# Performance work log

Measured on AMD Instinct MI355X. Metric: run time of the kernel, lower is better.

The kernel has to match this reference:

```python
import jax, jax.numpy as jnp
import numpy as np

N = 100000      # nodes
E = 1600000     # edges
IN_DIM = 500
HID = 64
OUT = 40
BN_EPS = 1e-5


def setup_inputs() -> dict:
    key = jax.random.key(0)
    ks = jax.random.split(key, 20)
    x = jax.random.normal(ks[0], (N, IN_DIM), dtype=jnp.float32)
    edge_index = jax.random.randint(ks[1], (2, E), 0, N, dtype=jnp.int64)

    def lin(k, fin, fout):
        return jax.random.normal(k, (fin, fout), dtype=jnp.float32) / np.sqrt(fin).astype(np.float32)

    inp = {
        "x": x,
        "edge_index": edge_index,
        "W1": lin(ks[2], IN_DIM, HID),
        "b1": jnp.zeros((HID,), jnp.float32),
        "g1": jnp.ones((HID,), jnp.float32),
        "be1": jnp.zeros((HID,), jnp.float32),
        "m1": 0.1 * jax.random.normal(ks[3], (HID,), jnp.float32),
        "v1": jax.random.uniform(ks[4], (HID,), jnp.float32, 0.5, 1.5),
        "W2": lin(ks[5], HID, HID),
        "b2": jnp.zeros((HID,), jnp.float32),
        "g2": jnp.ones((HID,), jnp.float32),
        "be2": jnp.zeros((HID,), jnp.float32),
        "m2": 0.1 * jax.random.normal(ks[6], (HID,), jnp.float32),
        "v2": jax.random.uniform(ks[7], (HID,), jnp.float32, 0.5, 1.5),
        "W3": lin(ks[8], HID, OUT),
        "b3": jnp.zeros((OUT,), jnp.float32),
    }
    return inp


def _gcn_conv(h, src, dst, deg_inv_sqrt, W, b):
    # PyG GCNConv (add_self_loops=True, normalize=True, eval math):
    # out = D^-1/2 (A + I) D^-1/2 (h @ W) + b
    h = h @ W                                    # [N, F]
    norm = deg_inv_sqrt[src] * deg_inv_sqrt[dst]  # [E]
    msg = h[src] * norm[:, None]                  # [E, F] gather
    agg = jax.ops.segment_sum(msg, dst, num_segments=N)  # scatter-add
    agg = agg + h * (deg_inv_sqrt * deg_inv_sqrt)[:, None]  # self-loop term
    return agg + b


def reference(x, edge_index, W1, b1, g1, be1, m1, v1,
              W2, b2, g2, be2, m2, v2, W3, b3):
    src, dst = edge_index[0], edge_index[1]
    # degree including self-loop
    deg = jax.ops.segment_sum(jnp.ones((E,), x.dtype), dst, num_segments=N) + 1.0
    deg_inv_sqrt = jax.lax.rsqrt(deg)

    def bn(h, g, be, m, v):
        return (h - m) * jax.lax.rsqrt(v + BN_EPS) * g + be

    h = _gcn_conv(x, src, dst, deg_inv_sqrt, W1, b1)
    h = jax.nn.relu(bn(h, g1, be1, m1, v1))
    # dropout: identity in eval mode
    h = _gcn_conv(h, src, dst, deg_inv_sqrt, W2, b2)
    h = jax.nn.relu(bn(h, g2, be2, m2, v2))
    out = _gcn_conv(h, src, dst, deg_inv_sqrt, W3, b3)
    return jax.nn.log_softmax(out, axis=1)
```

## Files before the change

kernel.cpp:

```cpp
#include <hip/hip_runtime.h>
#include <math.h>

#define N_NODES 100000
#define N_EDGES 1600000
#define IN_DIM  500
#define HID     64
#define OUT_DIM 40
#define BN_EPS  1e-5f
#define SCAN_NB 98
#define NTILE   6250

typedef __attribute__((ext_vector_type(8))) short bf16x8;
typedef __attribute__((ext_vector_type(4))) float f32x4;

static inline int cdiv(long a, int b) { return (int)((a + b - 1) / b); }

__device__ inline unsigned short f2bf_rne(float f) {
    unsigned int u = __float_as_uint(f);
    unsigned int r = (u + 0x7FFFu + ((u >> 16) & 1u)) >> 16;
    return (unsigned short)r;
}

__global__ void k_zero2(int* a, int* b) {
    int i = blockIdx.x * 256 + threadIdx.x;
    if (i < N_NODES) { a[i] = 0; b[i] = 0; }
}

__global__ void k_count_deg(const int* __restrict__ ei, int* degi) {
    int e = blockIdx.x * 256 + threadIdx.x;
    if (e < N_EDGES) atomicAdd(&degi[ei[N_EDGES + e]], 1);
}

__global__ void k_dis(const int* __restrict__ degi, float* dis) {
    int i = blockIdx.x * 256 + threadIdx.x;
    if (i < N_NODES) dis[i] = rsqrtf((float)degi[i] + 1.0f);
}

__global__ void k_scan1(const int* __restrict__ degi, int* __restrict__ rowptr,
                        int* __restrict__ blocksum) {
    __shared__ int sd[256];
    int tid = threadIdx.x;
    int base = blockIdx.x * 1024 + tid * 4;
    int v0 = (base + 0 < N_NODES) ? degi[base + 0] : 0;
    int v1 = (base + 1 < N_NODES) ? degi[base + 1] : 0;
    int v2 = (base + 2 < N_NODES) ? degi[base + 2] : 0;
    int v3 = (base + 3 < N_NODES) ? degi[base + 3] : 0;
    int s = v0 + v1 + v2 + v3;
    sd[tid] = s;
    __syncthreads();
    for (int off = 1; off < 256; off <<= 1) {
        int t = (tid >= off) ? sd[tid - off] : 0;
        __syncthreads();
        sd[tid] += t;
        __syncthreads();
    }
    int excl = sd[tid] - s;
    if (base + 0 < N_NODES) rowptr[base + 0] = excl;
    if (base + 1 < N_NODES) rowptr[base + 1] = excl + v0;
    if (base + 2 < N_NODES) rowptr[base + 2] = excl + v0 + v1;
    if (base + 3 < N_NODES) rowptr[base + 3] = excl + v0 + v1 + v2;
    if (tid == 255) blocksum[blockIdx.x] = sd[255];
}

__global__ void k_scan2(int* __restrict__ blocksum, int* __restrict__ blockbase) {
    __shared__ int sd[128];
    int tid = threadIdx.x;
    int v = (tid < SCAN_NB) ? blocksum[tid] : 0;
    sd[tid] = v;
    __syncthreads();
    for (int off = 1; off < 128; off <<= 1) {
        int t = (tid >= off) ? sd[tid - off] : 0;
        __syncthreads();
        sd[tid] += t;
        __syncthreads();
    }
    if (tid < SCAN_NB) blockbase[tid] = sd[tid] - v;
}

__global__ void k_scan3(int* __restrict__ rowptr, const int* __restrict__ blockbase) {
    int add = blockbase[blockIdx.x];
    int base = blockIdx.x * 1024 + threadIdx.x * 4;
#pragma unroll
    for (int i = 0; i < 4; ++i)
        if (base + i < N_NODES) rowptr[base + i] += add;
}

__global__ void k_permute(const int* __restrict__ ei, const int* __restrict__ rowptr,
                          int* __restrict__ cursor, const float* __restrict__ dis,
                          uint2* __restrict__ epack) {
    int e = blockIdx.x * 256 + threadIdx.x;
    if (e >= N_EDGES) return;
    int s = ei[e];
    int d = ei[N_EDGES + e];
    int pos = rowptr[d] + atomicAdd(&cursor[d], 1);
    epack[pos] = make_uint2((unsigned int)(s * 128),
                            __float_as_uint(dis[s] * dis[d]));
}

template <int K, int F, int T>
__global__ void k_convWp(const float* __restrict__ W, unsigned short* __restrict__ wb) {
    int idx = blockIdx.x * 256 + threadIdx.x;
    if (idx >= T * 2048) return;
    int j    = idx & 7;
    int lane = (idx >> 3) & 63;
    int q    = idx >> 9;
    int t    = q >> 2, nt = q & 3;
    int n = nt * 16 + (lane & 15);
    int k = t * 32 + ((lane >> 4) << 3) + j;
    float v = (k < K && n < F) ? W[(long)k * F + n] : 0.f;
    wb[idx] = f2bf_rne(v);
}

__global__ __launch_bounds__(256) void k_l1fused(
        const float* __restrict__ x,
        const unsigned short* __restrict__ wb,
        unsigned short* __restrict__ h) {
    __shared__ unsigned short l[16 * 520];
    const int rt = blockIdx.x;
    const int tid = threadIdx.x;

#pragma unroll
    for (int it = 0; it < 8; ++it) {
        int slot = it * 256 + tid;
        int row = slot >> 7, kq = slot & 127;
        float4 v = make_float4(0.f, 0.f, 0.f, 0.f);
        if (kq < 125)
            v = *reinterpret_cast<const float4*>(x + ((long)rt * 16 + row) * IN_DIM + kq * 4);
        unsigned int u0 = (unsigned int)f2bf_rne(v.x) | ((unsigned int)f2bf_rne(v.y) << 16);
        unsigned int u1 = (unsigned int)f2bf_rne(v.z) | ((unsigned int)f2bf_rne(v.w) << 16);
        *reinterpret_cast<uint2*>(&l[row * 520 + kq * 4]) = make_uint2(u0, u1);
    }
    __syncthreads();

    const int wid  = tid >> 6;
    const int lane = tid & 63;
    const int l15  = lane & 15;
    const int lhi  = lane >> 4;

    const bf16x8* bp = reinterpret_cast<const bf16x8*>(wb) + wid * 64 + lane;
    const unsigned short* arow = &l[l15 * 520 + lhi * 8];

    f32x4 acc = (f32x4){0.f, 0.f, 0.f, 0.f};
    bf16x8 ca = *reinterpret_cast<const bf16x8*>(arow);
    bf16x8 cb = bp[0];

#pragma unroll
    for (int t = 0; t < 16; ++t) {
        bf16x8 na, nb;
        if (t < 15) {
            na = *reinterpret_cast<const bf16x8*>(arow + (t + 1) * 32);
            nb = bp[(t + 1) * 256];
        }
        acc = __builtin_amdgcn_mfma_f32_16x16x32_bf16(ca, cb, acc, 0, 0, 0);
        if (t < 15) { ca = na; cb = nb; }
    }

#pragma unroll
    for (int rr = 0; rr < 4; ++rr) {
        long grow = (long)rt * 16 + lhi * 4 + rr;
        h[grow * 64 + wid * 16 + l15] = f2bf_rne(acc[rr]);
    }
}

template <int T>
__global__ __launch_bounds__(256) void k_gemm_packed(
        const unsigned short* __restrict__ xp,
        const unsigned short* __restrict__ wb,
        unsigned short* __restrict__ h) {
    const int tid  = threadIdx.x;
    const int wid  = tid >> 6;
    const int lane = tid & 63;
    const int rt   = blockIdx.x * 4 + wid;
    if (rt >= NTILE) return;

    const bf16x8* ap = reinterpret_cast<const bf16x8*>(xp) + (long)rt * T * 64 + lane;
    const bf16x8* bp = reinterpret_cast<const bf16x8*>(wb) + lane;

    f32x4 acc[4];
#pragma unroll
    for (int nt = 0; nt < 4; ++nt) acc[nt] = (f32x4){0.f, 0.f, 0.f, 0.f};

    bf16x8 ca = ap[0];
    bf16x8 cb0 = bp[0], cb1 = bp[64], cb2 = bp[128], cb3 = bp[192];

    for (int t = 0; t < T; ++t) {
        bf16x8 na, nb0, nb1, nb2, nb3;
        if (t + 1 < T) {
            na  = ap[(t + 1) * 64];
            nb0 = bp[((t + 1) * 4 + 0) * 64];
            nb1 = bp[((t + 1) * 4 + 1) * 64];
            nb2 = bp[((t + 1) * 4 + 2) * 64];
            nb3 = bp[((t + 1) * 4 + 3) * 64];
        }
        acc[0] = __builtin_amdgcn_mfma_f32_16x16x32_bf16(ca, cb0, acc[0], 0, 0, 0);
        acc[1] = __builtin_amdgcn_mfma_f32_16x16x32_bf16(ca, cb1, acc[1], 0, 0, 0);
        acc[2] = __builtin_amdgcn_mfma_f32_16x16x32_bf16(ca, cb2, acc[2], 0, 0, 0);
        acc[3] = __builtin_amdgcn_mfma_f32_16x16x32_bf16(ca, cb3, acc[3], 0, 0, 0);
        if (t + 1 < T) { ca = na; cb0 = nb0; cb1 = nb1; cb2 = nb2; cb3 = nb3; }
    }

    const int l15 = lane & 15, lhi = lane >> 4;
#pragma unroll
    for (int nt = 0; nt < 4; ++nt) {
        int coln = nt * 16 + l15;
#pragma unroll
        for (int rr = 0; rr < 4; ++rr) {
            long grow = (long)rt * 16 + lhi * 4 + rr;
            h[grow * 64 + coln] = f2bf_rne(acc[nt][rr]);
        }
    }
}

__global__ __launch_bounds__(256) void k_agg_bn_relu(
        const unsigned short* __restrict__ h, const int* __restrict__ rowptr,
        const int* __restrict__ degi, const uint2* __restrict__ epack,
        const float* __restrict__ dis,
        const float* __restrict__ bias, const float* __restrict__ g,
        const float* __restrict__ be, const float* __restrict__ m,
        const float* __restrict__ v, unsigned short* __restrict__ xp_out) {
    int node = blockIdx.x * 4 + (threadIdx.x >> 6);
    if (node >= N_NODES) return;
    const int lane = threadIdx.x & 63;
    const int e8 = lane >> 3, c8 = lane & 7;

    const int start = rowptr[node];
    const int cnt   = degi[node];
    const uint2* ep = epack + start;
    const char*  hb = (const char*)h + c8 * 16;

    float a[8] = {0.f, 0.f, 0.f, 0.f, 0.f, 0.f, 0.f, 0.f};

    auto batch = [&](int j) {
        int jj = j + e8;
        bool valid = jj < cnt;
        uint2 mv = ep[valid ? jj : 0];
        float w = valid ? __uint_as_float(mv.y) : 0.0f;
        uint4 hv = *(const uint4*)(hb + mv.x);
        a[0] += __uint_as_float(hv.x << 16) * w;
        a[1] += __uint_as_float(hv.x & 0xffff0000u) * w;
        a[2] += __uint_as_float(hv.y << 16) * w;
        a[3] += __uint_as_float(hv.y & 0xffff0000u) * w;
        a[4] += __uint_as_float(hv.z << 16) * w;
        a[5] += __uint_as_float(hv.z & 0xffff0000u) * w;
        a[6] += __uint_as_float(hv.w << 16) * w;
        a[7] += __uint_as_float(hv.w & 0xffff0000u) * w;
    };

    int j = 0;
    for (; j + 8 < cnt; j += 16) { batch(j); batch(j + 8); }
    if (j < cnt) batch(j);

#pragma unroll
    for (int i = 0; i < 8; ++i) {
        a[i] += __shfl_xor(a[i], 8);
        a[i] += __shfl_xor(a[i], 16);
        a[i] += __shfl_xor(a[i], 32);
    }

    if (e8 == 0) {
        float d = dis[node], d2 = d * d;
        uint4 sv = *(const uint4*)((const char*)h + (long)node * 128 + c8 * 16);
        float sf[8] = {
            __uint_as_float(sv.x << 16), __uint_as_float(sv.x & 0xffff0000u),
            __uint_as_float(sv.y << 16), __uint_as_float(sv.y & 0xffff0000u),
            __uint_as_float(sv.z << 16), __uint_as_float(sv.z & 0xffff0000u),
            __uint_as_float(sv.w << 16), __uint_as_float(sv.w & 0xffff0000u)};
        float4 bb0 = *(const float4*)(bias + c8 * 8), bb1 = *(const float4*)(bias + c8 * 8 + 4);
        float4 mm0 = *(const float4*)(m + c8 * 8),    mm1 = *(const float4*)(m + c8 * 8 + 4);
        float4 vv0 = *(const float4*)(v + c8 * 8),    vv1 = *(const float4*)(v + c8 * 8 + 4);
        float4 gg0 = *(const float4*)(g + c8 * 8),    gg1 = *(const float4*)(g + c8 * 8 + 4);
        float4 ee0 = *(const float4*)(be + c8 * 8),   ee1 = *(const float4*)(be + c8 * 8 + 4);
        float bbv[8] = {bb0.x, bb0.y, bb0.z, bb0.w, bb1.x, bb1.y, bb1.z, bb1.w};
        float mmv[8] = {mm0.x, mm0.y, mm0.z, mm0.w, mm1.x, mm1.y, mm1.z, mm1.w};
        float vvv[8] = {vv0.x, vv0.y, vv0.z, vv0.w, vv1.x, vv1.y, vv1.z, vv1.w};
        float ggv[8] = {gg0.x, gg0.y, gg0.z, gg0.w, gg1.x, gg1.y, gg1.z, gg1.w};
        float eev[8] = {ee0.x, ee0.y, ee0.z, ee0.w, ee1.x, ee1.y, ee1.z, ee1.w};

        unsigned int u[4];
#pragma unroll
        for (int p = 0; p < 4; ++p) {
            float r0 = a[2 * p]     + sf[2 * p]     * d2 + bbv[2 * p];
            float r1 = a[2 * p + 1] + sf[2 * p + 1] * d2 + bbv[2 * p + 1];
            r0 = fmaxf((r0 - mmv[2 * p])     * rsqrtf(vvv[2 * p]     + BN_EPS) * ggv[2 * p]     + eev[2 * p],     0.f);
            r1 = fmaxf((r1 - mmv[2 * p + 1]) * rsqrtf(vvv[2 * p + 1] + BN_EPS) * ggv[2 * p + 1] + eev[2 * p + 1], 0.f);
            u[p] = (unsigned int)f2bf_rne(r0) | ((unsigned int)f2bf_rne(r1) << 16);
        }

        int n16 = node & 15, rt2 = node >> 4;
        long base = (((long)rt2 * 2 + (c8 >> 2)) * 64 + (c8 & 3) * 16 + n16) * 8;
        *reinterpret_cast<uint4*>(xp_out + base) = make_uint4(u[0], u[1], u[2], u[3]);
    }
}

__global__ __launch_bounds__(256) void k_agg_lsm(
        const unsigned short* __restrict__ h, const int* __restrict__ rowptr,
        const int* __restrict__ degi, const uint2* __restrict__ epack,
        const float* __restrict__ dis,
        const float* __restrict__ bias, float* __restrict__ out) {
    int node = blockIdx.x * 4 + (threadIdx.x >> 6);
    if (node >= N_NODES) return;
    const int lane = threadIdx.x & 63;
    const int e8 = lane >> 3, c8 = lane & 7;

    const int start = rowptr[node];
    const int cnt   = degi[node];
    const uint2* ep = epack + start;
    const char*  hb = (const char*)h + c8 * 16;

    float a[8] = {0.f, 0.f, 0.f, 0.f, 0.f, 0.f, 0.f, 0.f};

    auto batch = [&](int j) {
        int jj = j + e8;
        bool valid = jj < cnt;
        uint2 mv = ep[valid ? jj : 0];
        float w = valid ? __uint_as_float(mv.y) : 0.0f;
        uint4 hv = *(const uint4*)(hb + mv.x);
        a[0] += __uint_as_float(hv.x << 16) * w;
        a[1] += __uint_as_float(hv.x & 0xffff0000u) * w;
        a[2] += __uint_as_float(hv.y << 16) * w;
        a[3] += __uint_as_float(hv.y & 0xffff0000u) * w;
        a[4] += __uint_as_float(hv.z << 16) * w;
        a[5] += __uint_as_float(hv.z & 0xffff0000u) * w;
        a[6] += __uint_as_float(hv.w << 16) * w;
        a[7] += __uint_as_float(hv.w & 0xffff0000u) * w;
    };

    int j = 0;
    for (; j + 8 < cnt; j += 16) { batch(j); batch(j + 8); }
    if (j < cnt) batch(j);

#pragma unroll
    for (int i = 0; i < 8; ++i) {
        a[i] += __shfl_xor(a[i], 8);
        a[i] += __shfl_xor(a[i], 16);
        a[i] += __shfl_xor(a[i], 32);
    }

    const bool ok = c8 < 5;
    float d = dis[node], d2 = d * d;
    uint4 sv = *(const uint4*)((const char*)h + (long)node * 128 + c8 * 16);
    float sf[8] = {
        __uint_as_float(sv.x << 16), __uint_as_float(sv.x & 0xffff0000u),
        __uint_as_float(sv.y << 16), __uint_as_float(sv.y & 0xffff0000u),
        __uint_as_float(sv.z << 16), __uint_as_float(sv.z & 0xffff0000u),
        __uint_as_float(sv.w << 16), __uint_as_float(sv.w & 0xffff0000u)};
    float vals[8];
    float mx = -INFINITY;
    if (ok) {
        float4 bb0 = *(const float4*)(bias + c8 * 8), bb1 = *(const float4*)(bias + c8 * 8 + 4);
        float bbv[8] = {bb0.x, bb0.y, bb0.z, bb0.w, bb1.x, bb1.y, bb1.z, bb1.w};
#pragma unroll
        for (int i = 0; i < 8; ++i) {
            vals[i] = a[i] + sf[i] * d2 + bbv[i];
            mx = fmaxf(mx, vals[i]);
        }
    }
#pragma unroll
    for (int o = 1; o < 8; o <<= 1) mx = fmaxf(mx, __shfl_xor(mx, o));
    float es = 0.f;
    if (ok) {
#pragma unroll
        for (int i = 0; i < 8; ++i) es += expf(vals[i] - mx);
    }
#pragma unroll
    for (int o = 1; o < 8; o <<= 1) es += __shfl_xor(es, o);
    float ls = logf(es);

    if (e8 == 0 && ok) {
        float* op = out + (long)node * 40 + c8 * 8;
        *(float4*)op = make_float4(vals[0] - mx - ls, vals[1] - mx - ls,
                                   vals[2] - mx - ls, vals[3] - mx - ls);
        *(float4*)(op + 4) = make_float4(vals[4] - mx - ls, vals[5] - mx - ls,
                                         vals[6] - mx - ls, vals[7] - mx - ls);
    }
}

extern "C" void kernel_launch(void* const* d_in, const int* in_sizes, int n_in,
                              void* d_out, int out_size, void* d_ws, size_t ws_size,
                              hipStream_t stream) {
    const float* x   = (const float*)d_in[0];
    const int*   ei  = (const int*)d_in[1];
    const float* W1  = (const float*)d_in[2];
    const float* b1  = (const float*)d_in[3];
    const float* g1  = (const float*)d_in[4];
    const float* be1 = (const float*)d_in[5];
    const float* m1  = (const float*)d_in[6];
    const float* v1  = (const float*)d_in[7];
    const float* W2  = (const float*)d_in[8];
    const float* b2  = (const float*)d_in[9];
    const float* g2  = (const float*)d_in[10];
    const float* be2 = (const float*)d_in[11];
    const float* m2  = (const float*)d_in[12];
    const float* v2  = (const float*)d_in[13];
    const float* W3  = (const float*)d_in[14];
    const float* b3  = (const float*)d_in[15];
    float* out = (float*)d_out;

    float* ws        = (float*)d_ws;
    float* dis       = ws;
    int*   degi      = (int*)(ws + 100096);
    int*   cursor    = (int*)(ws + 200192);
    int*   rowptr    = (int*)(ws + 300288);
    int*   blocksum  = (int*)(ws + 400384);
    int*   blockbase = (int*)(ws + 400512);
    uint2* epack     = (uint2*)(ws + 400640);
    unsigned short* bufH = (unsigned short*)(ws + 3600640);
    unsigned short* xp2  = (unsigned short*)(ws + 32400640);
    unsigned short* xp3  = (unsigned short*)(ws + 35600640);
    unsigned short* wb1  = (unsigned short*)(ws + 38800640);
    unsigned short* wb2  = (unsigned short*)(ws + 38817024);
    unsigned short* wb3  = (unsigned short*)(ws + 38819072);

    k_zero2<<<cdiv(N_NODES, 256), 256, 0, stream>>>(degi, cursor);
    k_count_deg<<<cdiv(N_EDGES, 256), 256, 0, stream>>>(ei, degi);
    k_dis<<<cdiv(N_NODES, 256), 256, 0, stream>>>(degi, dis);
    k_scan1<<<SCAN_NB, 256, 0, stream>>>(degi, rowptr, blocksum);
    k_scan2<<<1, 128, 0, stream>>>(blocksum, blockbase);
    k_scan3<<<SCAN_NB, 256, 0, stream>>>(rowptr, blockbase);
    k_permute<<<cdiv(N_EDGES, 256), 256, 0, stream>>>(ei, rowptr, cursor, dis, epack);

    k_convWp<IN_DIM, HID, 16><<<128, 256, 0, stream>>>(W1, wb1);
    k_convWp<HID, HID, 2><<<16, 256, 0, stream>>>(W2, wb2);
    k_convWp<HID, OUT_DIM, 2><<<16, 256, 0, stream>>>(W3, wb3);

    const int gemm_grid = cdiv(NTILE, 4);
    const int agg_grid  = cdiv(N_NODES, 4);

    k_l1fused<<<NTILE, 256, 0, stream>>>(x, wb1, bufH);
    k_agg_bn_relu<<<agg_grid, 256, 0, stream>>>(bufH, rowptr, degi, epack,
                                                dis, b1, g1, be1, m1, v1, xp2);

    k_gemm_packed<2><<<gemm_grid, 256, 0, stream>>>(xp2, wb2, bufH);
    k_agg_bn_relu<<<agg_grid, 256, 0, stream>>>(bufH, rowptr, degi, epack,
                                                dis, b2, g2, be2, m2, v2, xp3);

    k_gemm_packed<2><<<gemm_grid, 256, 0, stream>>>(xp3, wb3, bufH);
    k_agg_lsm<<<agg_grid, 256, 0, stream>>>(bufH, rowptr, degi, epack,
                                            dis, b3, out);
}
```

Before: 400.8 us.

## Switch bf16 to fp16 with packed half2 aggregation and fuse small setup kernels

Replaces the bf16 storage and MFMA with fp16 throughout. The edge aggregation now accumulates in packed half2 FMA instead of unpacking to fp32, and edge weights are stored as duplicated halves. Separately, the degree-inverse-sqrt computation is folded into the scan, the zeroing kernel becomes a memset, and the three weight-conversion launches are merged into one. This cuts ALU work in the gather loop and launch count, but fp16 accumulation over neighbours and the fp16 range limit on raw inputs add precision and overflow risk.

```diff
diff --git a/kernel.cpp b/kernel.cpp
--- a/kernel.cpp
+++ b/kernel.cpp
@@ -10,20 +10,19 @@
 #define SCAN_NB 98
 #define NTILE   6250
 
-typedef __attribute__((ext_vector_type(8))) short bf16x8;
+typedef _Float16 f16;
+typedef __attribute__((ext_vector_type(2))) _Float16 f16x2;
+typedef __attribute__((ext_vector_type(8))) _Float16 f16x8;
 typedef __attribute__((ext_vector_type(4))) float f32x4;
 
 static inline int cdiv(long a, int b) { return (int)((a + b - 1) / b); }
 
-__device__ inline unsigned short f2bf_rne(float f) {
-    unsigned int u = __float_as_uint(f);
-    unsigned int r = (u + 0x7FFFu + ((u >> 16) & 1u)) >> 16;
-    return (unsigned short)r;
-}
-
-__global__ void k_zero2(int* a, int* b) {
-    int i = blockIdx.x * 256 + threadIdx.x;
-    if (i < N_NODES) { a[i] = 0; b[i] = 0; }
+__device__ inline unsigned short f2h_bits(float f) {
+    f16 h = (f16)f;
+    return __builtin_bit_cast(unsigned short, h);
+}
+__device__ inline f16x2 bits2h2(unsigned int u) {
+    return __builtin_bit_cast(f16x2, u);
 }
 
 __global__ void k_count_deg(const int* __restrict__ ei, int* degi) {
@@ -31,13 +30,8 @@
     if (e < N_EDGES) atomicAdd(&degi[ei[N_EDGES + e]], 1);
 }
 
-__global__ void k_dis(const int* __restrict__ degi, float* dis) {
-    int i = blockIdx.x * 256 + threadIdx.x;
-    if (i < N_NODES) dis[i] = rsqrtf((float)degi[i] + 1.0f);
-}
-
 __global__ void k_scan1(const int* __restrict__ degi, int* __restrict__ rowptr,
-                        int* __restrict__ blocksum) {
+                        int* __restrict__ blocksum, float* __restrict__ dis) {
     __shared__ int sd[256];
     int tid = threadIdx.x;
     int base = blockIdx.x * 1024 + tid * 4;
@@ -45,6 +39,10 @@
     int v1 = (base + 1 < N_NODES) ? degi[base + 1] : 0;
     int v2 = (base + 2 < N_NODES) ? degi[base + 2] : 0;
     int v3 = (base + 3 < N_NODES) ? degi[base + 3] : 0;
+    if (base + 0 < N_NODES) dis[base + 0] = rsqrtf((float)v0 + 1.0f);
+    if (base + 1 < N_NODES) dis[base + 1] = rsqrtf((float)v1 + 1.0f);
+    if (base + 2 < N_NODES) dis[base + 2] = rsqrtf((float)v2 + 1.0f);
+    if (base + 3 < N_NODES) dis[base + 3] = rsqrtf((float)v3 + 1.0f);
     int s = v0 + v1 + v2 + v3;
     sd[tid] = s;
     __syncthreads();
@@ -93,14 +91,12 @@
     int s = ei[e];
     int d = ei[N_EDGES + e];
     int pos = rowptr[d] + atomicAdd(&cursor[d], 1);
-    epack[pos] = make_uint2((unsigned int)(s * 128),
-                            __float_as_uint(dis[s] * dis[d]));
-}
-
-template <int K, int F, int T>
-__global__ void k_convWp(const float* __restrict__ W, unsigned short* __restrict__ wb) {
-    int idx = blockIdx.x * 256 + threadIdx.x;
-    if (idx >= T * 2048) return;
+    unsigned int hb = f2h_bits(dis[s] * dis[d]);
+    epack[pos] = make_uint2((unsigned int)(s * 128), (hb << 16) | hb);
+}
+
+__device__ inline void convW_one(const float* W, unsigned short* wb,
+                                 int idx, int K, int F) {
     int j    = idx & 7;
     int lane = (idx >> 3) & 63;
     int q    = idx >> 9;
@@ -108,7 +104,22 @@
     int n = nt * 16 + (lane & 15);
     int k = t * 32 + ((lane >> 4) << 3) + j;
     float v = (k < K && n < F) ? W[(long)k * F + n] : 0.f;
-    wb[idx] = f2bf_rne(v);
+    wb[idx] = f2h_bits(v);
+}
+
+__global__ void k_convall(const float* __restrict__ W1, const float* __restrict__ W2,
+                          const float* __restrict__ W3,
+                          unsigned short* __restrict__ wb1,
+                          unsigned short* __restrict__ wb2,
+                          unsigned short* __restrict__ wb3) {
+    int idx = blockIdx.x * 256 + threadIdx.x;
+    if (idx < 32768) {
+        convW_one(W1, wb1, idx, IN_DIM, HID);
+    } else if (idx < 36864) {
+        convW_one(W2, wb2, idx - 32768, HID, HID);
+    } else {
+        convW_one(W3, wb3, idx - 36864, HID, OUT_DIM);
+    }
 }
 
 __global__ __launch_bounds__(256) void k_l1fused(
@@ -126,8 +137,8 @@
         float4 v = make_float4(0.f, 0.f, 0.f, 0.f);
         if (kq < 125)
             v = *reinterpret_cast<const float4*>(x + ((long)rt * 16 + row) * IN_DIM + kq * 4);
-        unsigned int u0 = (unsigned int)f2bf_rne(v.x) | ((unsigned int)f2bf_rne(v.y) << 16);
-        unsigned int u1 = (unsigned int)f2bf_rne(v.z) | ((unsigned int)f2bf_rne(v.w) << 16);
+        unsigned int u0 = (unsigned int)f2h_bits(v.x) | ((unsigned int)f2h_bits(v.y) << 16);
+        unsigned int u1 = (unsigned int)f2h_bits(v.z) | ((unsigned int)f2h_bits(v.w) << 16);
         *reinterpret_cast<uint2*>(&l[row * 520 + kq * 4]) = make_uint2(u0, u1);
     }
     __syncthreads();
@@ -137,28 +148,28 @@
     const int l15  = lane & 15;
     const int lhi  = lane >> 4;
 
-    const bf16x8* bp = reinterpret_cast<const bf16x8*>(wb) + wid * 64 + lane;
+    const f16x8* bp = reinterpret_cast<const f16x8*>(wb) + wid * 64 + lane;
     const unsigned short* arow = &l[l15 * 520 + lhi * 8];
 
     f32x4 acc = (f32x4){0.f, 0.f, 0.f, 0.f};
-    bf16x8 ca = *reinterpret_cast<const bf16x8*>(arow);
-    bf16x8 cb = bp[0];
+    f16x8 ca = *reinterpret_cast<const f16x8*>(arow);
+    f16x8 cb = bp[0];
 
 #pragma unroll
     for (int t = 0; t < 16; ++t) {
-        bf16x8 na, nb;
+        f16x8 na, nb;
         if (t < 15) {
-            na = *reinterpret_cast<const bf16x8*>(arow + (t + 1) * 32);
+            na = *reinterpret_cast<const f16x8*>(arow + (t + 1) * 32);
             nb = bp[(t + 1) * 256];
         }
-        acc = __builtin_amdgcn_mfma_f32_16x16x32_bf16(ca, cb, acc, 0, 0, 0);
+        acc = __builtin_amdgcn_mfma_f32_16x16x32_f16(ca, cb, acc, 0, 0, 0);
         if (t < 15) { ca = na; cb = nb; }
     }
 
 #pragma unroll
     for (int rr = 0; rr < 4; ++rr) {
         long grow = (long)rt * 16 + lhi * 4 + rr;
-        h[grow * 64 + wid * 16 + l15] = f2bf_rne(acc[rr]);
+        h[grow * 64 + wid * 16 + l15] = f2h_bits(acc[rr]);
     }
 }
 
@@ -173,18 +184,18 @@
     const int rt   = blockIdx.x * 4 + wid;
     if (rt >= NTILE) return;
 
-    const bf16x8* ap = reinterpret_cast<const bf16x8*>(xp) + (long)rt * T * 64 + lane;
-    const bf16x8* bp = reinterpret_cast<const bf16x8*>(wb) + lane;
+    const f16x8* ap = reinterpret_cast<const f16x8*>(xp) + (long)rt * T * 64 + lane;
+    const f16x8* bp = reinterpret_cast<const f16x8*>(wb) + lane;
 
     f32x4 acc[4];
 #pragma unroll
     for (int nt = 0; nt < 4; ++nt) acc[nt] = (f32x4){0.f, 0.f, 0.f, 0.f};
 
-    bf16x8 ca = ap[0];
-    bf16x8 cb0 = bp[0], cb1 = bp[64], cb2 = bp[128], cb3 = bp[192];
+    f16x8 ca = ap[0];
+    f16x8 cb0 = bp[0], cb1 = bp[64], cb2 = bp[128], cb3 = bp[192];
 
     for (int t = 0; t < T; ++t) {
-        bf16x8 na, nb0, nb1, nb2, nb3;
+        f16x8 na, nb0, nb1, nb2, nb3;
         if (t + 1 < T) {
             na  = ap[(t + 1) * 64];
             nb0 = bp[((t + 1) * 4 + 0) * 64];
@@ -192,10 +203,10 @@
             nb2 = bp[((t + 1) * 4 + 2) * 64];
             nb3 = bp[((t + 1) * 4 + 3) * 64];
         }
-        acc[0] = __builtin_amdgcn_mfma_f32_16x16x32_bf16(ca, cb0, acc[0], 0, 0, 0);
-        acc[1] = __builtin_amdgcn_mfma_f32_16x16x32_bf16(ca, cb1, acc[1], 0, 0, 0);
-        acc[2] = __builtin_amdgcn_mfma_f32_16x16x32_bf16(ca, cb2, acc[2], 0, 0, 0);
-        acc[3] = __builtin_amdgcn_mfma_f32_16x16x32_bf16(ca, cb3, acc[3], 0, 0, 0);
+        acc[0] = __builtin_amdgcn_mfma_f32_16x16x32_f16(ca, cb0, acc[0], 0, 0, 0);
+        acc[1] = __builtin_amdgcn_mfma_f32_16x16x32_f16(ca, cb1, acc[1], 0, 0, 0);
+        acc[2] = __builtin_amdgcn_mfma_f32_16x16x32_f16(ca, cb2, acc[2], 0, 0, 0);
+        acc[3] = __builtin_amdgcn_mfma_f32_16x16x32_f16(ca, cb3, acc[3], 0, 0, 0);
         if (t + 1 < T) { ca = na; cb0 = nb0; cb1 = nb1; cb2 = nb2; cb3 = nb3; }
     }
 
@@ -206,7 +217,7 @@
 #pragma unroll
         for (int rr = 0; rr < 4; ++rr) {
             long grow = (long)rt * 16 + lhi * 4 + rr;
-            h[grow * 64 + coln] = f2bf_rne(acc[nt][rr]);
+            h[grow * 64 + coln] = f2h_bits(acc[nt][rr]);
         }
     }
 }
@@ -228,22 +239,18 @@
     const uint2* ep = epack + start;
     const char*  hb = (const char*)h + c8 * 16;
 
-    float a[8] = {0.f, 0.f, 0.f, 0.f, 0.f, 0.f, 0.f, 0.f};
+    f16x2 a[4] = {(f16x2)0, (f16x2)0, (f16x2)0, (f16x2)0};
 
     auto batch = [&](int j) {
         int jj = j + e8;
         bool valid = jj < cnt;
         uint2 mv = ep[valid ? jj : 0];
-        float w = valid ? __uint_as_float(mv.y) : 0.0f;
+        f16x2 w2 = bits2h2(valid ? mv.y : 0u);
         uint4 hv = *(const uint4*)(hb + mv.x);
-        a[0] += __uint_as_float(hv.x << 16) * w;
-        a[1] += __uint_as_float(hv.x & 0xffff0000u) * w;
-        a[2] += __uint_as_float(hv.y << 16) * w;
-        a[3] += __uint_as_float(hv.y & 0xffff0000u) * w;
-        a[4] += __uint_as_float(hv.z << 16) * w;
-        a[5] += __uint_as_float(hv.z & 0xffff0000u) * w;
-        a[6] += __uint_as_float(hv.w << 16) * w;
-        a[7] += __uint_as_float(hv.w & 0xffff0000u) * w;
+        a[0] += bits2h2(hv.x) * w2;
+        a[1] += bits2h2(hv.y) * w2;
+        a[2] += bits2h2(hv.z) * w2;
+        a[3] += bits2h2(hv.w) * w2;
     };
 
     int j = 0;
@@ -251,20 +258,23 @@
     if (j < cnt) batch(j);
 
 #pragma unroll
-    for (int i = 0; i < 8; ++i) {
-        a[i] += __shfl_xor(a[i], 8);
-        a[i] += __shfl_xor(a[i], 16);
-        a[i] += __shfl_xor(a[i], 32);
+    for (int off = 8; off < 64; off <<= 1) {
+#pragma unroll
+        for (int i = 0; i < 4; ++i) {
+            unsigned int u = __builtin_bit_cast(unsigned int, a[i]);
+            a[i] += bits2h2((unsigned int)__shfl_xor((int)u, off));
+        }
     }
 
     if (e8 == 0) {
         float d = dis[node], d2 = d * d;
         uint4 sv = *(const uint4*)((const char*)h + (long)node * 128 + c8 * 16);
-        float sf[8] = {
-            __uint_as_float(sv.x << 16), __uint_as_float(sv.x & 0xffff0000u),
-            __uint_as_float(sv.y << 16), __uint_as_float(sv.y & 0xffff0000u),
-            __uint_as_float(sv.z << 16), __uint_as_float(sv.z & 0xffff0000u),
-            __uint_as_float(sv.w << 16), __uint_as_float(sv.w & 0xffff0000u)};
+        f16x2 s01 = bits2h2(sv.x), s23 = bits2h2(sv.y);
+        f16x2 s45 = bits2h2(sv.z), s67 = bits2h2(sv.w);
+        float av[8] = {(float)a[0][0], (float)a[0][1], (float)a[1][0], (float)a[1][1],
+                       (float)a[2][0], (float)a[2][1], (float)a[3][0], (float)a[3][1]};
+        float sf[8] = {(float)s01[0], (float)s01[1], (float)s23[0], (float)s23[1],
+                       (float)s45[0], (float)s45[1], (float)s67[0], (float)s67[1]};
         float4 bb0 = *(const float4*)(bias + c8 * 8), bb1 = *(const float4*)(bias + c8 * 8 + 4);
         float4 mm0 = *(const float4*)(m + c8 * 8),    mm1 = *(const float4*)(m + c8 * 8 + 4);
         float4 vv0 = *(const float4*)(v + c8 * 8),    vv1 = *(const float4*)(v + c8 * 8 + 4);
@@ -279,11 +289,11 @@
         unsigned int u[4];
 #pragma unroll
         for (int p = 0; p < 4; ++p) {
-            float r0 = a[2 * p]     + sf[2 * p]     * d2 + bbv[2 * p];
-            float r1 = a[2 * p + 1] + sf[2 * p + 1] * d2 + bbv[2 * p + 1];
+            float r0 = av[2 * p]     + sf[2 * p]     * d2 + bbv[2 * p];
+            float r1 = av[2 * p + 1] + sf[2 * p + 1] * d2 + bbv[2 * p + 1];
             r0 = fmaxf((r0 - mmv[2 * p])     * rsqrtf(vvv[2 * p]     + BN_EPS) * ggv[2 * p]     + eev[2 * p],     0.f);
             r1 = fmaxf((r1 - mmv[2 * p + 1]) * rsqrtf(vvv[2 * p + 1] + BN_EPS) * ggv[2 * p + 1] + eev[2 * p + 1], 0.f);
-            u[p] = (unsigned int)f2bf_rne(r0) | ((unsigned int)f2bf_rne(r1) << 16);
+            u[p] = (unsigned int)f2h_bits(r0) | ((unsigned int)f2h_bits(r1) << 16);
         }
 
         int n16 = node & 15, rt2 = node >> 4;
@@ -307,22 +317,18 @@
     const uint2* ep = epack + start;
     const char*  hb = (const char*)h + c8 * 16;
 
-    float a[8] = {0.f, 0.f, 0.f, 0.f, 0.f, 0.f, 0.f, 0.f};
+    f16x2 a[4] = {(f16x2)0, (f16x2)0, (f16x2)0, (f16x2)0};
 
     auto batch = [&](int j) {
         int jj = j + e8;
         bool valid = jj < cnt;
         uint2 mv = ep[valid ? jj : 0];
-        float w = valid ? __uint_as_float(mv.y) : 0.0f;
+        f16x2 w2 = bits2h2(valid ? mv.y : 0u);
         uint4 hv = *(const uint4*)(hb + mv.x);
-        a[0] += __uint_as_float(hv.x << 16) * w;
-        a[1] += __uint_as_float(hv.x & 0xffff0000u) * w;
-        a[2] += __uint_as_float(hv.y << 16) * w;
-        a[3] += __uint_as_float(hv.y & 0xffff0000u) * w;
-        a[4] += __uint_as_float(hv.z << 16) * w;
-        a[5] += __uint_as_float(hv.z & 0xffff0000u) * w;
-        a[6] += __uint_as_float(hv.w << 16) * w;
-        a[7] += __uint_as_float(hv.w & 0xffff0000u) * w;
+        a[0] += bits2h2(hv.x) * w2;
+        a[1] += bits2h2(hv.y) * w2;
+        a[2] += bits2h2(hv.z) * w2;
+        a[3] += bits2h2(hv.w) * w2;
     };
 
     int j = 0;
@@ -330,20 +336,23 @@
     if (j < cnt) batch(j);
 
 #pragma unroll
-    for (int i = 0; i < 8; ++i) {
-        a[i] += __shfl_xor(a[i], 8);
-        a[i] += __shfl_xor(a[i], 16);
-        a[i] += __shfl_xor(a[i], 32);
+    for (int off = 8; off < 64; off <<= 1) {
+#pragma unroll
+        for (int i = 0; i < 4; ++i) {
+            unsigned int u = __builtin_bit_cast(unsigned int, a[i]);
+            a[i] += bits2h2((unsigned int)__shfl_xor((int)u, off));
+        }
     }
 
     const bool ok = c8 < 5;
     float d = dis[node], d2 = d * d;
     uint4 sv = *(const uint4*)((const char*)h + (long)node * 128 + c8 * 16);
-    float sf[8] = {
-        __uint_as_float(sv.x << 16), __uint_as_float(sv.x & 0xffff0000u),
-        __uint_as_float(sv.y << 16), __uint_as_float(sv.y & 0xffff0000u),
-        __uint_as_float(sv.z << 16), __uint_as_float(sv.z & 0xffff0000u),
-        __uint_as_float(sv.w << 16), __uint_as_float(sv.w & 0xffff0000u)};
+    f16x2 s01 = bits2h2(sv.x), s23 = bits2h2(sv.y);
+    f16x2 s45 = bits2h2(sv.z), s67 = bits2h2(sv.w);
+    float av[8] = {(float)a[0][0], (float)a[0][1], (float)a[1][0], (float)a[1][1],
+                   (float)a[2][0], (float)a[2][1], (float)a[3][0], (float)a[3][1]};
+    float sf[8] = {(float)s01[0], (float)s01[1], (float)s23[0], (float)s23[1],
+                   (float)s45[0], (float)s45[1], (float)s67[0], (float)s67[1]};
     float vals[8];
     float mx = -INFINITY;
     if (ok) {
@@ -351,7 +360,7 @@
         float bbv[8] = {bb0.x, bb0.y, bb0.z, bb0.w, bb1.x, bb1.y, bb1.z, bb1.w};
 #pragma unroll
         for (int i = 0; i < 8; ++i) {
-            vals[i] = a[i] + sf[i] * d2 + bbv[i];
+            vals[i] = av[i] + sf[i] * d2 + bbv[i];
             mx = fmaxf(mx, vals[i]);
         }
     }
@@ -411,17 +420,14 @@
     unsigned short* wb2  = (unsigned short*)(ws + 38817024);
     unsigned short* wb3  = (unsigned short*)(ws + 38819072);
 
-    k_zero2<<<cdiv(N_NODES, 256), 256, 0, stream>>>(degi, cursor);
+    hipMemsetAsync(degi, 0, 2 * 100096 * sizeof(int), stream);
     k_count_deg<<<cdiv(N_EDGES, 256), 256, 0, stream>>>(ei, degi);
-    k_dis<<<cdiv(N_NODES, 256), 256, 0, stream>>>(degi, dis);
-    k_scan1<<<SCAN_NB, 256, 0, stream>>>(degi, rowptr, blocksum);
+    k_scan1<<<SCAN_NB, 256, 0, stream>>>(degi, rowptr, blocksum, dis);
     k_scan2<<<1, 128, 0, stream>>>(blocksum, blockbase);
     k_scan3<<<SCAN_NB, 256, 0, stream>>>(rowptr, blockbase);
     k_permute<<<cdiv(N_EDGES, 256), 256, 0, stream>>>(ei, rowptr, cursor, dis, epack);
 
-    k_convWp<IN_DIM, HID, 16><<<128, 256, 0, stream>>>(W1, wb1);
-    k_convWp<HID, HID, 2><<<16, 256, 0, stream>>>(W2, wb2);
-    k_convWp<HID, OUT_DIM, 2><<<16, 256, 0, stream>>>(W3, wb3);
+    k_convall<<<160, 256, 0, stream>>>(W1, W2, W3, wb1, wb2, wb3);
 
     const int gemm_grid = cdiv(NTILE, 4);
     const int agg_grid  = cdiv(N_NODES, 4);
```

Measured after the change: 394.5 us. About the same (-1.6%).
